# Kernel tuning notes

Hardware: AMD Instinct MI355X
Metric: run time of the kernel (lower is better)

The kernel has to match this reference:

```python
import jax, jax.numpy as jnp
import numpy as np

K = 9          # temporal window (kernel_size)
PAD = (K - 1) // 2
BN_EPS = 1e-5


def setup_inputs() -> dict:
    key = jax.random.key(0)
    ks = jax.random.split(key, 9)
    N, Cin, Cout, T, V = 16, 64, 128, 256, 25
    return {
        "x": jax.random.normal(ks[0], (N, Cin, T, V), jnp.float32),
        "conv_w": jax.random.normal(ks[1], (Cout, Cin), jnp.float32) * (1.0 / np.sqrt(Cin)),
        "conv_b": jax.random.normal(ks[2], (Cout,), jnp.float32) * 0.01,
        "gamma": jax.random.uniform(ks[3], (Cout,), jnp.float32, 0.5, 1.5),
        "beta": jax.random.normal(ks[4], (Cout,), jnp.float32) * 0.1,
        "run_mean": jax.random.normal(ks[5], (Cout,), jnp.float32) * 0.1,
        "run_var": jax.random.uniform(ks[6], (Cout,), jnp.float32, 0.5, 1.5),
        "att0": jnp.full((1, Cout, 1, K), 1.0 / K, jnp.float32),
        "A": jax.random.uniform(ks[7], (V, V), jnp.float32),
        "keep_prob": 1,
    }


def reference(x, conv_w, conv_b, gamma, beta, run_mean, run_var, att0, A, keep_prob):
    # 1x1 conv (pointwise channel mix); AvgPool2d((1,1)) is identity for stride=1
    x = jnp.einsum("nctv,oc->notv", x, conv_w) + conv_b[None, :, None, None]
    # BatchNorm2d (eval mode: running stats)
    scale = gamma / jnp.sqrt(run_var + BN_EPS)
    x = x * scale[None, :, None, None] + (beta - run_mean * scale)[None, :, None, None]
    N, C, T, V = x.shape
    # UnfoldTemporalWindows: zero-pad T, gather K temporal shifts -> (N, C, T, K, V)
    xp = jnp.pad(x, ((0, 0), (0, 0), (PAD, PAD), (0, 0)))
    upfold = jnp.stack([xp[:, :, u:u + T, :] for u in range(K)], axis=3)
    # local attention: score each window position against the center frame
    scores = jnp.einsum("nctv,nctuv->nctu", x, upfold) / V
    attn = jax.nn.softmax(scores, axis=-1) + att0
    out = jnp.einsum("nctuv,nctu->nctv", upfold, attn)
    # dropS / dropT are identity at keep_prob == 1 (inference)
    return out
```

## Files before the change

kernel.cpp:

```cpp
#include <hip/hip_runtime.h>
#include <hip/hip_bf16.h>

#define CIN   64
#define COUT  128
#define TT    256
#define VV    25
#define TV    (TT * VV)
#define KW    9
#define PAD   4

typedef __attribute__((ext_vector_type(8))) short short8;
typedef __attribute__((ext_vector_type(4))) float f32x4;

__device__ __forceinline__ unsigned f2b(float f) {
    unsigned u = __builtin_bit_cast(unsigned, f);
    return (u + 0x7FFFu + ((u >> 16) & 1u)) >> 16;
}
__device__ __forceinline__ float lof(unsigned u) {
    return __builtin_bit_cast(float, u << 16);
}
__device__ __forceinline__ float hif(unsigned u) {
    return __builtin_bit_cast(float, u & 0xffff0000u);
}
__device__ __forceinline__ int swz(int row, int cbyte) {
    return row * 128 + ((cbyte & ~15) ^ ((row & 7) << 4)) + (cbyte & 15);
}

__global__ __launch_bounds__(256) void conv_mfma(
    const float* __restrict__ x, const float* __restrict__ w,
    const float* __restrict__ cb, const float* __restrict__ gamma,
    const float* __restrict__ beta, const float* __restrict__ rm,
    const float* __restrict__ rv, unsigned short* __restrict__ y)
{
    __shared__ __align__(16) unsigned short Wl[COUT * 64];
    __shared__ __align__(16) unsigned short Xl[128 * 64];
    __shared__ float sc[COUT];
    __shared__ float of[COUT];

    const int pc  = blockIdx.x;
    const int n   = blockIdx.y;
    const int tid = threadIdx.x;
    const int posbase = pc * 128;

    if (tid < COUT) {
        const float s = gamma[tid] * rsqrtf(rv[tid] + 1e-5f);
        sc[tid] = s;
        of[tid] = cb[tid] * s + beta[tid] - rm[tid] * s;
    }
    for (int idx = tid; idx < 2048; idx += 256) {
        const int c4 = idx & 15, o = idx >> 4;
        const f32x4 wv = *(const f32x4*)(w + o * 64 + c4 * 4);
        uint2 pk;
        pk.x = f2b(wv.x) | (f2b(wv.y) << 16);
        pk.y = f2b(wv.z) | (f2b(wv.w) << 16);
        *(uint2*)((char*)Wl + swz(o, c4 * 8)) = pk;
    }
    for (int idx = tid; idx < 2048; idx += 256) {
        const int pos = idx & 127, c4 = idx >> 7;
        const float* xp = x + (size_t)n * CIN * TV + (size_t)(c4 * 4) * TV + posbase + pos;
        const float a0 = xp[0], a1 = xp[TV], a2 = xp[2 * TV], a3 = xp[3 * TV];
        uint2 pk;
        pk.x = f2b(a0) | (f2b(a1) << 16);
        pk.y = f2b(a2) | (f2b(a3) << 16);
        *(uint2*)((char*)Xl + swz(pos, c4 * 8)) = pk;
    }
    __syncthreads();

    const int wv_ = tid >> 6, lane = tid & 63;
    const int lr = lane & 15, lh = lane >> 4;

    short8 bw[2][2];
#pragma unroll
    for (int nn = 0; nn < 2; ++nn)
#pragma unroll
        for (int kh = 0; kh < 2; ++kh)
            bw[nn][kh] = *(const short8*)((const char*)Wl +
                              swz(wv_ * 32 + nn * 16 + lr, kh * 64 + lh * 16));

    f32x4 acc[8][2];
#pragma unroll
    for (int m = 0; m < 8; ++m)
#pragma unroll
        for (int nn = 0; nn < 2; ++nn) acc[m][nn] = (f32x4){0.f, 0.f, 0.f, 0.f};

#pragma unroll
    for (int m = 0; m < 8; ++m) {
        const int prow = m * 16 + lr;
        const short8 a0 = *(const short8*)((const char*)Xl + swz(prow, lh * 16));
        const short8 a1 = *(const short8*)((const char*)Xl + swz(prow, 64 + lh * 16));
#pragma unroll
        for (int nn = 0; nn < 2; ++nn) {
            acc[m][nn] = __builtin_amdgcn_mfma_f32_16x16x32_bf16(a0, bw[nn][0], acc[m][nn], 0, 0, 0);
            acc[m][nn] = __builtin_amdgcn_mfma_f32_16x16x32_bf16(a1, bw[nn][1], acc[m][nn], 0, 0, 0);
        }
    }

#pragma unroll
    for (int nn = 0; nn < 2; ++nn) {
        const int o = wv_ * 32 + nn * 16 + lr;
        const float s = sc[o], f = of[o];
        unsigned short* yb = y + (size_t)(n * COUT + o) * TV + posbase + lh * 4;
#pragma unroll
        for (int m = 0; m < 8; ++m) {
            const f32x4 a = acc[m][nn];
            uint2 pk;
            pk.x = f2b(a[0] * s + f) | (f2b(a[1] * s + f) << 16);
            pk.y = f2b(a[2] * s + f) | (f2b(a[3] * s + f) << 16);
            *(uint2*)(yb + m * 16) = pk;
        }
    }
}

#define LOADROW(lr_, dst)                                                   \
    {                                                                       \
        const int ub_ = 7 * (lr_);                                          \
        const uint2 r0_ = tl2[ub_],     r1_ = tl2[ub_ + 1];                 \
        const uint2 r2_ = tl2[ub_ + 2], r3_ = tl2[ub_ + 3];                 \
        const uint2 r4_ = tl2[ub_ + 4], r5_ = tl2[ub_ + 5];                 \
        const unsigned l_ = tlu[14 * (lr_) + 12];                           \
        (dst)[0]  = lof(r0_.x); (dst)[1]  = hif(r0_.x);                     \
        (dst)[2]  = lof(r0_.y); (dst)[3]  = hif(r0_.y);                     \
        (dst)[4]  = lof(r1_.x); (dst)[5]  = hif(r1_.x);                     \
        (dst)[6]  = lof(r1_.y); (dst)[7]  = hif(r1_.y);                     \
        (dst)[8]  = lof(r2_.x); (dst)[9]  = hif(r2_.x);                     \
        (dst)[10] = lof(r2_.y); (dst)[11] = hif(r2_.y);                     \
        (dst)[12] = lof(r3_.x); (dst)[13] = hif(r3_.x);                     \
        (dst)[14] = lof(r3_.y); (dst)[15] = hif(r3_.y);                     \
        (dst)[16] = lof(r4_.x); (dst)[17] = hif(r4_.x);                     \
        (dst)[18] = lof(r4_.y); (dst)[19] = hif(r4_.y);                     \
        (dst)[20] = lof(r5_.x); (dst)[21] = hif(r5_.x);                     \
        (dst)[22] = lof(r5_.y); (dst)[23] = hif(r5_.y);                     \
        (dst)[24] = lof(l_);                                                \
    }

__global__ __launch_bounds__(256) void attn_kernel(
    const unsigned short* __restrict__ y, const float* __restrict__ att0,
    float* __restrict__ out)
{
    __shared__ __align__(16) float sm[TV];
    __shared__ float a0s[KW];

    uint4* tl4 = (uint4*)sm;
    const uint2* tl2 = (const uint2*)sm;
    const unsigned* tlu = (const unsigned*)sm;
    unsigned* tlw = (unsigned*)sm;

    const int nc  = blockIdx.x;
    const int c   = nc & (COUT - 1);
    const int tid = threadIdx.x;

    if (tid < KW) a0s[tid] = att0[c * KW + tid];

    if (tid < 28) {
        const int i = (tid < 14) ? tid : (896 + tid);
        tl4[i] = make_uint4(0, 0, 0, 0);
    }

    {
        const unsigned* ygu = (const unsigned*)(y + (size_t)nc * TV);
        const int t = tid;
        const int s0 = (25 * t) >> 1;
        const int odd = t & 1;
        unsigned u[14];
#pragma unroll
        for (int i = 0; i < 14; ++i) u[i] = ygu[min(s0 + i, 3199)];
        unsigned* dst = tlw + 14 * (t + 4);
#pragma unroll
        for (int d = 0; d < 13; ++d) {
            const unsigned shifted = (u[d] >> 16) | (u[d + 1] << 16);
            dst[d] = odd ? shifted : u[d];
        }
    }
    __syncthreads();

    const int t = tid;

    float q[25];
    LOADROW(t + 4, q);

    float osm[25], oa0[25];
    float den;
    {
        float d0 = 0.f, d1 = 0.f;
#pragma unroll
        for (int v = 0; v < 12; ++v)  d0 = fmaf(q[v], q[v], d0);
#pragma unroll
        for (int v = 12; v < 25; ++v) d1 = fmaf(q[v], q[v], d1);
        const float e = __expf((d0 + d1) * (1.f / 25.f));
        den = e;
        const float a = a0s[4];
#pragma unroll
        for (int v = 0; v < 25; ++v) { osm[v] = e * q[v]; oa0[v] = a * q[v]; }
    }

#pragma unroll
    for (int j = 0; j < KW; ++j) {
        if (j == 4) continue;
        float row[25];
        LOADROW(t + j, row);
        float d0 = 0.f, d1 = 0.f;
#pragma unroll
        for (int v = 0; v < 12; ++v)  d0 = fmaf(row[v], q[v], d0);
#pragma unroll
        for (int v = 12; v < 25; ++v) d1 = fmaf(row[v], q[v], d1);
        const float e = __expf((d0 + d1) * (1.f / 25.f));
        den += e;
        const float a = a0s[j];
#pragma unroll
        for (int v = 0; v < 25; ++v) {
            osm[v] = fmaf(e, row[v], osm[v]);
            oa0[v] = fmaf(a, row[v], oa0[v]);
        }
    }

    const float inv = 1.f / den;

    __syncthreads();
    {
        float* dst = &sm[t * 25];
#pragma unroll
        for (int v = 0; v < 25; ++v) dst[v] = fmaf(osm[v], inv, oa0[v]);
    }
    __syncthreads();

    {
        float4* og = (float4*)(out + (size_t)nc * TV);
        const float4* sm4 = (const float4*)sm;
#pragma unroll
        for (int i = 0; i < 7; ++i) {
            const int ci = tid + i * 256;
            if (ci < TV / 4) og[ci] = sm4[ci];
        }
    }
}

extern "C" void kernel_launch(void* const* d_in, const int* in_sizes, int n_in,
                              void* d_out, int out_size, void* d_ws, size_t ws_size,
                              hipStream_t stream)
{
    const float* x     = (const float*)d_in[0];
    const float* w     = (const float*)d_in[1];
    const float* cb    = (const float*)d_in[2];
    const float* gamma = (const float*)d_in[3];
    const float* beta  = (const float*)d_in[4];
    const float* rm    = (const float*)d_in[5];
    const float* rv    = (const float*)d_in[6];
    const float* att0  = (const float*)d_in[7];
    float* out = (float*)d_out;
    unsigned short* y = (unsigned short*)d_ws;

    dim3 gA(TV / 128, 16);
    conv_mfma<<<gA, 256, 0, stream>>>(x, w, cb, gamma, beta, rm, rv, y);

    dim3 gB(16 * COUT);
    attn_kernel<<<gB, 256, 0, stream>>>(y, att0, out);
}
```

Measured before the change: 44.54 us.

## Split attention accumulation across two threads per time step

The attention kernel now launches 512 threads per block, with two threads per time step. One thread accumulates the softmax-weighted window sum and the other accumulates the att0-weighted sum. The two partial results go to separate shared-memory halves and are added during the store to global memory. This halves the per-thread accumulator registers and FMA chain to raise occupancy and parallelism, at the cost of duplicated score computation, double the shared memory (about 51 KB), and an extra combine pass.

```diff
diff --git a/kernel.cpp b/kernel.cpp
--- a/kernel.cpp
+++ b/kernel.cpp
@@ -133,11 +133,11 @@
         (dst)[24] = lof(l_);                                                \
     }
 
-__global__ __launch_bounds__(256) void attn_kernel(
+__global__ __launch_bounds__(512) void attn_kernel(
     const unsigned short* __restrict__ y, const float* __restrict__ att0,
     float* __restrict__ out)
 {
-    __shared__ __align__(16) float sm[TV];
+    __shared__ __align__(16) float sm[2 * TV];
     __shared__ float a0s[KW];
 
     uint4* tl4 = (uint4*)sm;
@@ -148,6 +148,8 @@
     const int nc  = blockIdx.x;
     const int c   = nc & (COUT - 1);
     const int tid = threadIdx.x;
+    const int t    = tid >> 1;
+    const int role = tid & 1;
 
     if (tid < KW) a0s[tid] = att0[c * KW + tid];
 
@@ -158,44 +160,41 @@
 
     {
         const unsigned* ygu = (const unsigned*)(y + (size_t)nc * TV);
-        const int t = tid;
         const int s0 = (25 * t) >> 1;
         const int odd = t & 1;
-        unsigned u[14];
-#pragma unroll
-        for (int i = 0; i < 14; ++i) u[i] = ygu[min(s0 + i, 3199)];
         unsigned* dst = tlw + 14 * (t + 4);
-#pragma unroll
-        for (int d = 0; d < 13; ++d) {
-            const unsigned shifted = (u[d] >> 16) | (u[d + 1] << 16);
-            dst[d] = odd ? shifted : u[d];
-        }
-    }
-    __syncthreads();
-
-    const int t = tid;
+        if (role == 0) {
+            unsigned u[8];
+#pragma unroll
+            for (int i = 0; i < 8; ++i) u[i] = ygu[min(s0 + i, 3199)];
+#pragma unroll
+            for (int d = 0; d < 7; ++d) {
+                const unsigned shifted = (u[d] >> 16) | (u[d + 1] << 16);
+                dst[d] = odd ? shifted : u[d];
+            }
+        } else {
+            unsigned u[7];
+#pragma unroll
+            for (int i = 0; i < 7; ++i) u[i] = ygu[min(s0 + 7 + i, 3199)];
+#pragma unroll
+            for (int d = 7; d < 13; ++d) {
+                const unsigned shifted = (u[d - 7] >> 16) | (u[d - 6] << 16);
+                dst[d] = odd ? shifted : u[d - 7];
+            }
+        }
+    }
+    __syncthreads();
 
     float q[25];
     LOADROW(t + 4, q);
 
-    float osm[25], oa0[25];
-    float den;
-    {
-        float d0 = 0.f, d1 = 0.f;
-#pragma unroll
-        for (int v = 0; v < 12; ++v)  d0 = fmaf(q[v], q[v], d0);
-#pragma unroll
-        for (int v = 12; v < 25; ++v) d1 = fmaf(q[v], q[v], d1);
-        const float e = __expf((d0 + d1) * (1.f / 25.f));
-        den = e;
-        const float a = a0s[4];
-#pragma unroll
-        for (int v = 0; v < 25; ++v) { osm[v] = e * q[v]; oa0[v] = a * q[v]; }
-    }
+    float acc[25];
+#pragma unroll
+    for (int v = 0; v < 25; ++v) acc[v] = 0.f;
+    float den = 0.f;
 
 #pragma unroll
     for (int j = 0; j < KW; ++j) {
-        if (j == 4) continue;
         float row[25];
         LOADROW(t + j, row);
         float d0 = 0.f, d1 = 0.f;
@@ -205,31 +204,33 @@
         for (int v = 12; v < 25; ++v) d1 = fmaf(row[v], q[v], d1);
         const float e = __expf((d0 + d1) * (1.f / 25.f));
         den += e;
-        const float a = a0s[j];
-#pragma unroll
-        for (int v = 0; v < 25; ++v) {
-            osm[v] = fmaf(e, row[v], osm[v]);
-            oa0[v] = fmaf(a, row[v], oa0[v]);
-        }
+        const float coef = role ? a0s[j] : e;
+#pragma unroll
+        for (int v = 0; v < 25; ++v) acc[v] = fmaf(coef, row[v], acc[v]);
     }
 
     const float inv = 1.f / den;
 
     __syncthreads();
     {
-        float* dst = &sm[t * 25];
-#pragma unroll
-        for (int v = 0; v < 25; ++v) dst[v] = fmaf(osm[v], inv, oa0[v]);
+        float* dst = &sm[role * TV + t * 25];
+        const float scale = role ? 1.f : inv;
+#pragma unroll
+        for (int v = 0; v < 25; ++v) dst[v] = acc[v] * scale;
     }
     __syncthreads();
 
     {
         float4* og = (float4*)(out + (size_t)nc * TV);
-        const float4* sm4 = (const float4*)sm;
-#pragma unroll
-        for (int i = 0; i < 7; ++i) {
-            const int ci = tid + i * 256;
-            if (ci < TV / 4) og[ci] = sm4[ci];
+        const float4* smA = (const float4*)sm;
+        const float4* smB = (const float4*)(sm + TV);
+#pragma unroll
+        for (int i = 0; i < 4; ++i) {
+            const int ci = tid + i * 512;
+            if (ci < TV / 4) {
+                const float4 a = smA[ci], b = smB[ci];
+                og[ci] = make_float4(a.x + b.x, a.y + b.y, a.z + b.z, a.w + b.w);
+            }
         }
     }
 }
@@ -253,5 +254,5 @@
     conv_mfma<<<gA, 256, 0, stream>>>(x, w, cb, gamma, beta, rm, rv, y);
 
     dim3 gB(16 * COUT);
-    attn_kernel<<<gB, 256, 0, stream>>>(y, att0, out);
-}
+    attn_kernel<<<gB, 512, 0, stream>>>(y, att0, out);
+}
```

Result: slower. 68.11 us (+52.9%).

## Compute temporal-window attention with bf16 MFMA banded score and output matmuls

Applied to the files above, without the earlier changes.

Replaces the per-thread scalar FP32 dot products and weighted sums over the 9-frame window with banded 16x32 MFMA tiles. Scores come from center rows times neighbor rows. The softmax-plus-att0 coefficients are written as a bf16 band matrix and multiplied against a transposed copy of the rows. New swizzled and transposed LDS layouts are built during staging. This trades scalar VALU work and register pressure for MFMA work that is partly wasted on the band, adds extra LDS traffic, leaves only 16 of 64 lanes doing the softmax, and rounds the coefficients to bf16.

```diff
diff --git a/kernel.cpp b/kernel.cpp
--- a/kernel.cpp
+++ b/kernel.cpp
@@ -8,6 +8,12 @@
 #define TV    (TT * VV)
 #define KW    9
 #define PAD   4
+
+#define YT_BASE 16896
+#define YTSTR   280
+#define S_BASE  30896
+#define CF_BASE 40112
+#define SMEM_SZ 44208
 
 typedef __attribute__((ext_vector_type(8))) short short8;
 typedef __attribute__((ext_vector_type(4))) float f32x4;
@@ -111,49 +117,31 @@
     }
 }
 
-#define LOADROW(lr_, dst)                                                   \
-    {                                                                       \
-        const int ub_ = 7 * (lr_);                                          \
-        const uint2 r0_ = tl2[ub_],     r1_ = tl2[ub_ + 1];                 \
-        const uint2 r2_ = tl2[ub_ + 2], r3_ = tl2[ub_ + 3];                 \
-        const uint2 r4_ = tl2[ub_ + 4], r5_ = tl2[ub_ + 5];                 \
-        const unsigned l_ = tlu[14 * (lr_) + 12];                           \
-        (dst)[0]  = lof(r0_.x); (dst)[1]  = hif(r0_.x);                     \
-        (dst)[2]  = lof(r0_.y); (dst)[3]  = hif(r0_.y);                     \
-        (dst)[4]  = lof(r1_.x); (dst)[5]  = hif(r1_.x);                     \
-        (dst)[6]  = lof(r1_.y); (dst)[7]  = hif(r1_.y);                     \
-        (dst)[8]  = lof(r2_.x); (dst)[9]  = hif(r2_.x);                     \
-        (dst)[10] = lof(r2_.y); (dst)[11] = hif(r2_.y);                     \
-        (dst)[12] = lof(r3_.x); (dst)[13] = hif(r3_.x);                     \
-        (dst)[14] = lof(r3_.y); (dst)[15] = hif(r3_.y);                     \
-        (dst)[16] = lof(r4_.x); (dst)[17] = hif(r4_.x);                     \
-        (dst)[18] = lof(r4_.y); (dst)[19] = hif(r4_.y);                     \
-        (dst)[20] = lof(r5_.x); (dst)[21] = hif(r5_.x);                     \
-        (dst)[22] = lof(r5_.y); (dst)[23] = hif(r5_.y);                     \
-        (dst)[24] = lof(l_);                                                \
-    }
-
 __global__ __launch_bounds__(256) void attn_kernel(
     const unsigned short* __restrict__ y, const float* __restrict__ att0,
     float* __restrict__ out)
 {
-    __shared__ __align__(16) float sm[TV];
+    __shared__ __align__(16) char smem[SMEM_SZ];
     __shared__ float a0s[KW];
 
-    uint4* tl4 = (uint4*)sm;
-    const uint2* tl2 = (const uint2*)sm;
-    const unsigned* tlu = (const unsigned*)sm;
-    unsigned* tlw = (unsigned*)sm;
+    unsigned* yw = (unsigned*)smem;
+    unsigned short* ytr = (unsigned short*)(smem + YT_BASE);
 
     const int nc  = blockIdx.x;
     const int c   = nc & (COUT - 1);
     const int tid = threadIdx.x;
+    const int lane = tid & 63, w = tid >> 6;
 
     if (tid < KW) a0s[tid] = att0[c * KW + tid];
 
-    if (tid < 28) {
-        const int i = (tid < 14) ? tid : (896 + tid);
-        tl4[i] = make_uint4(0, 0, 0, 0);
+    if (tid < 8) {
+        const int r = (tid < 4) ? tid : 256 + tid;
+#pragma unroll
+        for (int d = 0; d < 16; ++d) yw[r * 16 + d] = 0;
+    }
+    if (tid < 200) {
+        const int v = tid >> 3, k = tid & 7;
+        ((unsigned*)ytr)[v * 140 + (k < 2 ? k : 128 + k)] = 0;
     }
 
     {
@@ -164,68 +152,111 @@
         unsigned u[14];
 #pragma unroll
         for (int i = 0; i < 14; ++i) u[i] = ygu[min(s0 + i, 3199)];
-        unsigned* dst = tlw + 14 * (t + 4);
+        unsigned rd[13];
 #pragma unroll
         for (int d = 0; d < 13; ++d) {
-            const unsigned shifted = (u[d] >> 16) | (u[d + 1] << 16);
-            dst[d] = odd ? shifted : u[d];
-        }
-    }
-    __syncthreads();
-
-    const int t = tid;
-
-    float q[25];
-    LOADROW(t + 4, q);
-
-    float osm[25], oa0[25];
-    float den;
+            const unsigned sh = (u[d] >> 16) | (u[d + 1] << 16);
+            rd[d] = odd ? sh : u[d];
+        }
+        rd[12] &= 0xffffu;
+        const int r = t + 4;
+        const int rx = (r & 3) ^ ((r >> 2) & 3);
+#pragma unroll
+        for (int d = 0; d < 13; ++d)
+            yw[r * 16 + ((((d >> 2) ^ rx) << 2) | (d & 3))] = rd[d];
+#pragma unroll
+        for (int d = 13; d < 16; ++d)
+            yw[r * 16 + (((3 ^ rx) << 2) | (d & 3))] = 0;
+#pragma unroll
+        for (int v = 0; v < 25; ++v) {
+            const unsigned dd = rd[v >> 1];
+            ytr[v * YTSTR + r] = (unsigned short)((v & 1) ? (dd >> 16) : (dd & 0xffffu));
+        }
+    }
     {
-        float d0 = 0.f, d1 = 0.f;
-#pragma unroll
-        for (int v = 0; v < 12; ++v)  d0 = fmaf(q[v], q[v], d0);
-#pragma unroll
-        for (int v = 12; v < 25; ++v) d1 = fmaf(q[v], q[v], d1);
-        const float e = __expf((d0 + d1) * (1.f / 25.f));
-        den = e;
-        const float a = a0s[4];
-#pragma unroll
-        for (int v = 0; v < 25; ++v) { osm[v] = e * q[v]; oa0[v] = a * q[v]; }
-    }
-
-#pragma unroll
-    for (int j = 0; j < KW; ++j) {
-        if (j == 4) continue;
-        float row[25];
-        LOADROW(t + j, row);
-        float d0 = 0.f, d1 = 0.f;
-#pragma unroll
-        for (int v = 0; v < 12; ++v)  d0 = fmaf(row[v], q[v], d0);
-#pragma unroll
-        for (int v = 12; v < 25; ++v) d1 = fmaf(row[v], q[v], d1);
-        const float e = __expf((d0 + d1) * (1.f / 25.f));
-        den += e;
-        const float a = a0s[j];
-#pragma unroll
-        for (int v = 0; v < 25; ++v) {
-            osm[v] = fmaf(e, row[v], osm[v]);
-            oa0[v] = fmaf(a, row[v], oa0[v]);
-        }
-    }
-
-    const float inv = 1.f / den;
-
-    __syncthreads();
-    {
-        float* dst = &sm[t * 25];
-#pragma unroll
-        for (int v = 0; v < 25; ++v) dst[v] = fmaf(osm[v], inv, oa0[v]);
-    }
-    __syncthreads();
-
+        uint4* cfz = (uint4*)(smem + CF_BASE + w * 1024);
+        cfz[lane] = make_uint4(0, 0, 0, 0);
+    }
+    __syncthreads();
+
+    float* sS = (float*)(smem + S_BASE + w * 2304);
+    char* cfb = smem + CF_BASE + w * 1024;
+    const int lr16 = lane & 15, q = lane >> 4;
+
+    f32x4 ok[4][2];
+
+#pragma unroll
+    for (int ch = 0; ch < 4; ++ch) {
+        const int t0 = (w * 4 + ch) * 16;
+
+        short8 af, b1, b2;
+        {
+            const int ra = t0 + 4 + lr16;
+            af = *(const short8*)(smem + ra * 64 + ((q ^ (ra & 3) ^ ((ra >> 2) & 3)) << 4));
+            const int rb1 = t0 + lr16;
+            b1 = *(const short8*)(smem + rb1 * 64 + ((q ^ (rb1 & 3) ^ ((rb1 >> 2) & 3)) << 4));
+            const int rb2 = t0 + 16 + lr16;
+            b2 = *(const short8*)(smem + rb2 * 64 + ((q ^ (rb2 & 3) ^ ((rb2 >> 2) & 3)) << 4));
+        }
+        f32x4 s1 = (f32x4){0.f, 0.f, 0.f, 0.f}, s2 = (f32x4){0.f, 0.f, 0.f, 0.f};
+        s1 = __builtin_amdgcn_mfma_f32_16x16x32_bf16(af, b1, s1, 0, 0, 0);
+        s2 = __builtin_amdgcn_mfma_f32_16x16x32_bf16(af, b2, s2, 0, 0, 0);
+
+#pragma unroll
+        for (int r = 0; r < 4; ++r) {
+            sS[(q * 4 + r) * 36 + lr16]      = s1[r];
+            sS[(q * 4 + r) * 36 + 16 + lr16] = s2[r];
+        }
+
+        if (lane < 16) {
+            const int m = lane;
+            float e[9], den = 0.f;
+#pragma unroll
+            for (int j = 0; j < 9; ++j) {
+                e[j] = __expf(sS[m * 36 + m + j] * (1.f / 25.f));
+                den += e[j];
+            }
+            const float inv = 1.f / den;
+            const int mx = (m & 3) ^ ((m >> 2) & 3);
+#pragma unroll
+            for (int j = 0; j < 9; ++j) {
+                const int n = m + j;
+                const float cf = fmaf(e[j], inv, a0s[j]);
+                *(unsigned short*)(cfb + m * 64 + ((((n >> 3) ^ mx) << 4) | ((n & 7) << 1)))
+                    = (unsigned short)f2b(cf);
+            }
+        }
+
+        short8 ac, bv1, bv2;
+        {
+            const int mx = (lr16 & 3) ^ ((lr16 >> 2) & 3);
+            ac  = *(const short8*)(cfb + lr16 * 64 + ((q ^ mx) << 4));
+            bv1 = *(const short8*)((char*)ytr + lr16 * 560 + (t0 + q * 8) * 2);
+            bv2 = *(const short8*)((char*)ytr + (16 + lr16) * 560 + (t0 + q * 8) * 2);
+        }
+        f32x4 o1 = (f32x4){0.f, 0.f, 0.f, 0.f}, o2 = (f32x4){0.f, 0.f, 0.f, 0.f};
+        o1 = __builtin_amdgcn_mfma_f32_16x16x32_bf16(ac, bv1, o1, 0, 0, 0);
+        o2 = __builtin_amdgcn_mfma_f32_16x16x32_bf16(ac, bv2, o2, 0, 0, 0);
+        ok[ch][0] = o1;
+        ok[ch][1] = o2;
+    }
+    __syncthreads();
+
+    float* ov = (float*)smem;
+#pragma unroll
+    for (int ch = 0; ch < 4; ++ch) {
+        const int rowb = (w * 4 + ch) * 16 + q * 4;
+#pragma unroll
+        for (int r = 0; r < 4; ++r) {
+            ov[(rowb + r) * 25 + lr16] = ok[ch][0][r];
+            if (lr16 < 9)
+                ov[(rowb + r) * 25 + 16 + lr16] = ok[ch][1][r];
+        }
+    }
+    __syncthreads();
     {
         float4* og = (float4*)(out + (size_t)nc * TV);
-        const float4* sm4 = (const float4*)sm;
+        const float4* sm4 = (const float4*)smem;
 #pragma unroll
         for (int i = 0; i < 7; ++i) {
             const int ci = tid + i * 256;
```

Result: no change. 44.64 us (+0.2%).
